# Optimization experiments

Measured on AMD Instinct MI355X. Metric: run time of the kernel, lower is better.

Reference implementation:

```python
import math
import jax, jax.numpy as jnp
import numpy as np


def setup_inputs() -> dict:
    key = jax.random.key(0)
    k1, k2 = jax.random.split(key)
    x = jax.random.normal(k1, (32, 3, 64, 64), dtype=jnp.float32)   # (B,C,H,W)
    y = jax.random.normal(k2, (512, 3, 64, 64), dtype=jnp.float32)  # (N,C,H,W)
    return {"x": x, "y": y}


def reference(x, y):
    # Faithful to torch rfft/irfft with normalized=True (unitary / 'ortho' scaling).
    B, C, H, W = x.shape
    scale = math.sqrt(H * W)  # self.N in the torch module
    X = jnp.fft.rfft2(x, norm="ortho")  # (B,C,H,W//2+1) complex
    Y = jnp.fft.rfft2(y, norm="ortho")  # (N,C,H,W//2+1) complex
    # conj(X) . Y summed over channels, fused as one complex contraction
    G = jnp.einsum("bchw,nchw->bnhw", jnp.conj(X), Y)  # (B,N,H,W//2+1)
    g = jnp.fft.irfft2(G, s=(H, W), norm="ortho") * scale  # (B,N,H,W)
    m = jnp.max(g, axis=(-2, -1))  # MaxPool2d(kernel=input_size) -> (B,N)
    xx = jnp.linalg.norm(x.reshape(B, -1), axis=-1)[:, None]  # (B,1)
    yy = jnp.linalg.norm(y.reshape(y.shape[0], -1), axis=-1)[None, :]  # (1,N)
    return m / xx / yy
```

## Files before the change

### kernel.cpp

```cpp
#include <hip/hip_runtime.h>
#include <math.h>

#define FBINS 2112
#define CSC 68

typedef float cplx __attribute__((ext_vector_type(2)));
typedef __fp16 half2v __attribute__((ext_vector_type(2)));
#define MK2(a,b) (cplx){(float)(a), (float)(b)}

__device__ __forceinline__ cplx shufxy(cplx a){ return __builtin_shufflevector(a, a, 1, 0); }
template<int S> __device__ __forceinline__ cplx imul(cplx a){
    return (S > 0) ? shufxy(a) * MK2(-1.f, 1.f) : shufxy(a) * MK2(1.f, -1.f);
}
template<int S> __device__ __forceinline__ cplx cmul_tw(cplx a, cplx w){
    cplx ws = shufxy(w);
    return (S > 0) ? a.x*w + a.y*(ws*MK2(-1.f, 1.f))
                   : a.x*(w*MK2(1.f, -1.f)) + a.y*ws;
}

__device__ __forceinline__ unsigned pack16(float a, float b){
    half2v h = __builtin_amdgcn_cvt_pkrtz(a, b);
    return __builtin_bit_cast(unsigned, h);
}
__device__ __forceinline__ half2v h2(unsigned u){ return __builtin_bit_cast(half2v, u); }
__device__ __forceinline__ float fdot2(half2v a, half2v b, float c){
#if __has_builtin(__builtin_amdgcn_fdot2)
    return __builtin_amdgcn_fdot2(a, b, c, false);
#else
    return c + (float)a.x*(float)b.x + (float)a.y*(float)b.y;
#endif
}

template<int S>
__device__ __forceinline__ void dft8(cplx v[8]) {
    const float C = 0.70710678118654752440f;
    cplx t0=v[0]+v[4], t4=v[0]-v[4];
    cplx t1=v[1]+v[5], t5=v[1]-v[5];
    cplx t2=v[2]+v[6], t6=v[2]-v[6];
    cplx t3=v[3]+v[7], t7=v[3]-v[7];
    cplx u0=t0+t2, u2=t0-t2;
    cplx u1=t1+t3, u3=t1-t3;
    v[0]=u0+u1; v[4]=u0-u1;
    cplx m3=imul<S>(u3);
    v[2]=u2+m3; v[6]=u2-m3;
    cplx z0=t4;
    cplx z1 = C*(t5 + imul<S>(t5));
    cplx z2 = imul<S>(t6);
    cplx z3 = C*(imul<S>(t7) - t7);
    cplx w0=z0+z2, w2=z0-z2;
    cplx w1=z1+z3, w3=z1-z3;
    v[1]=w0+w1; v[5]=w0-w1;
    cplx mb=imul<S>(w3);
    v[3]=w2+mb; v[7]=w2-mb;
}

template<int S>
__device__ __forceinline__ void fft64_from_regs(
    cplx v[8], cplx* __restrict__ mem, int base, int j, const cplx wj[7])
{
    dft8<S>(v);
    #pragma unroll
    for (int k=1;k<8;++k) v[k] = cmul_tw<S>(v[k], wj[k-1]);
    #pragma unroll
    for (int k=0;k<8;++k) mem[base + 8*j + (k^j)] = v[k];
    #pragma unroll
    for (int n=0;n<8;++n) v[n] = mem[base + 8*n + (j^n)];
    dft8<S>(v);
}

__device__ __forceinline__ void init_twtable(cplx* TWS, int tid){
    if (tid < 56) {
        int jj = tid / 7, kk = tid - 7*jj + 1;
        float sn, cs;
        sincosf(6.283185307179586f * (float)(jj*kk) / 64.0f, &sn, &cs);
        TWS[tid] = MK2(cs, sn);
    }
}
__device__ __forceinline__ void load_tw(const cplx* TWS, int j, cplx wj[7]){
    #pragma unroll
    for (int k=0;k<7;++k) wj[k] = TWS[j*7+k];
}

__global__ __launch_bounds__(256) void fwd_fft_kernel(
    const float* __restrict__ in, unsigned* __restrict__ oA,
    unsigned* __restrict__ oB, float* __restrict__ pn, int dual)
{
    __shared__ __align__(16) cplx CL[32*CSC + 64];
    __shared__ cplx TWS[56];
    __shared__ float red[4];
    const int tid = threadIdx.x, G = tid>>3, j = tid&7;

    init_twtable(TWS, tid);

    const float* img = in + (size_t)blockIdx.x * 4096;

    cplx wj[7];
    {
        cplx v[8];
        float ns = 0.f;
        #pragma unroll
        for (int nn=0;nn<8;++nn){ int w=8*nn+j;
            float a = img[64*G + w], c = img[64*(G+32) + w];
            v[nn] = MK2(a, c);
            ns = fmaf(a, a, ns); ns = fmaf(c, c, ns); }
        #pragma unroll
        for (int off = 32; off; off >>= 1) ns += __shfl_xor(ns, off);
        if ((tid & 63) == 0) red[tid >> 6] = ns;
        __syncthreads();
        load_tw(TWS, j, wj);
        int base = CSC*G;
        fft64_from_regs<-1>(v, CL, base, j, wj);
        #pragma unroll
        for (int k=0;k<8;++k) CL[base + j + 8*k] = v[k];
    }
    __syncthreads();

    {
        cplx v[8];
        if (G == 0) {
            #pragma unroll
            for (int nn=0;nn<8;++nn){
                int r=8*nn+j, p=r&31, hi=r>>5;
                cplx a0  = CL[CSC*p + 0];
                cplx a32 = CL[CSC*p + 32];
                v[nn] = hi ? MK2(a0.y, a32.y) : MK2(a0.x, a32.x);
            }
        } else {
            const int c = G;
            #pragma unroll
            for (int nn=0;nn<8;++nn){
                int r=8*nn+j, p=r&31, hi=r>>5;
                cplx A  = CL[CSC*p + c];
                cplx Bm = CL[CSC*p + 64 - c];
                if (!hi) v[nn] = 0.5f*(A + Bm*MK2(1.f,-1.f));
                else     v[nn] = 0.5f*(shufxy(A)*MK2(1.f,-1.f) + shufxy(Bm));
            }
        }
        __syncthreads();
        int base = CSC*G;
        fft64_from_regs<-1>(v, CL, base, j, wj);
        #pragma unroll
        for (int k=0;k<8;++k) CL[base + j + 8*k] = v[k];
    }
    __syncthreads();

    unsigned* a = oA + (size_t)blockIdx.x * FBINS;
    unsigned* bq = dual ? (oB + (size_t)blockIdx.x * FBINS) : nullptr;
    for (int i = tid; i < FBINS; i += 256) {
        int wp = i>>6, h = i&63;
        cplx r;
        if (wp == 0) {
            int h2i = (64-h)&63;
            cplx av = CL[h], bb = CL[h2i];
            r = 0.5f*(av + bb*MK2(1.f,-1.f));
        } else if (wp == 32) {
            int h2i = (64-h)&63;
            cplx av = CL[h], bb = CL[h2i];
            r = 0.5f*(shufxy(av)*MK2(1.f,-1.f) + shufxy(bb));
        } else {
            r = CL[CSC*wp + h];
        }
        a[i] = pack16(r.x, r.y);
        if (dual) bq[i] = pack16(-r.y, r.x);
    }
    if (tid == 0) pn[blockIdx.x] = red[0] + red[1] + red[2] + red[3];
}

__global__ __launch_bounds__(256) void corr_kernel(
    const unsigned* __restrict__ Xa, const unsigned* __restrict__ Xb,
    const unsigned* __restrict__ Yh,
    const float* __restrict__ px, const float* __restrict__ py,
    float* __restrict__ out)
{
    __shared__ __align__(16) cplx CL[32*CSC + 64];
    __shared__ cplx TWS[56];
    __shared__ float red[4];
    const int tid = threadIdx.x, G = tid>>3, j = tid&7;

    const int blk = blockIdx.x;
    const int xcd = blk & 7, idx = blk >> 3;
    const int n = xcd*64 + (idx & 63);
    const int b = idx >> 6;

    init_twtable(TWS, tid);

    const float x2 = px[3*b] + px[3*b+1] + px[3*b+2];
    const float y2 = py[3*n] + py[3*n+1] + py[3*n+2];
    const float dinv = rsqrtf(x2 * y2) * (1.0f/4096.0f);

    const uint4* pXa = (const uint4*)Xa + (size_t)b * 3 * 528;
    const uint4* pXb = (const uint4*)Xb + (size_t)b * 3 * 528;
    const uint4* pY  = (const uint4*)Yh + (size_t)n * 3 * 528;
    #pragma unroll
    for (int t = 0; t < 3; ++t) {
        int i = tid + (t<<8);
        if (i < 528) {
            float r0=0,i0=0,r1=0,i1=0,r2=0,i2=0,r3=0,i3=0;
            #pragma unroll
            for (int ch = 0; ch < 3; ++ch) {
                uint4 ua = pXa[ch*528 + i];
                uint4 ub = pXb[ch*528 + i];
                uint4 uy = pY [ch*528 + i];
                r0 = fdot2(h2(ua.x), h2(uy.x), r0);  i0 = fdot2(h2(ub.x), h2(uy.x), i0);
                r1 = fdot2(h2(ua.y), h2(uy.y), r1);  i1 = fdot2(h2(ub.y), h2(uy.y), i1);
                r2 = fdot2(h2(ua.z), h2(uy.z), r2);  i2 = fdot2(h2(ub.z), h2(uy.z), i2);
                r3 = fdot2(h2(ua.w), h2(uy.w), r3);  i3 = fdot2(h2(ub.w), h2(uy.w), i3);
            }
            int bin = 4*i;
            int s = CSC*(bin>>6) + (bin&63);
            *(float4*)&CL[s]   = make_float4(r0,i0,r1,i1);
            *(float4*)&CL[s+2] = make_float4(r2,i2,r3,i3);
        }
    }
    __syncthreads();

    cplx wj[7]; load_tw(TWS, j, wj);

    {
        cplx v[8];
        int base = CSC*G;
        if (G == 0) {
            #pragma unroll
            for (int nn=0;nn<8;++nn){
                int h = 8*nn + j;
                cplx a = CL[h];
                cplx c = CL[CSC*32 + h];
                v[nn] = a + imul<1>(c);
            }
        } else {
            #pragma unroll
            for (int nn=0;nn<8;++nn) v[nn] = CL[base + 8*nn + j];
        }
        fft64_from_regs<1>(v, CL, base, j, wj);
        #pragma unroll
        for (int k=0;k<8;++k) CL[base + j + 8*k] = v[k];
    }
    __syncthreads();

    float m = -3.4e38f;
    {
        const int r1 = G, r2 = G + 32;
        cplx v[8];
        if (j == 0) {
            cplx a = CL[r1], c = CL[r2];
            v[0] = MK2(a.x, c.x);
            v[4] = MK2(a.y, c.y);
        } else {
            cplx a = CL[CSC*j + r1], c = CL[CSC*j + r2];
            v[0] = a + imul<1>(c);
            int w2 = 32 - j;
            cplx a2 = CL[CSC*w2 + r1], c2 = CL[CSC*w2 + r2];
            v[4] = a2*MK2(1.f,-1.f) + shufxy(c2);
        }
        #pragma unroll
        for (int nn=1; nn<4; ++nn) {
            int w = 8*nn + j;
            cplx a = CL[CSC*w + r1], c = CL[CSC*w + r2];
            v[nn] = a + imul<1>(c);
        }
        #pragma unroll
        for (int nn=5; nn<8; ++nn) {
            int w2 = 64 - (8*nn + j);
            cplx a = CL[CSC*w2 + r1], c = CL[CSC*w2 + r2];
            v[nn] = a*MK2(1.f,-1.f) + shufxy(c);
        }
        __syncthreads();
        fft64_from_regs<1>(v, CL, CSC*G, j, wj);
        #pragma unroll
        for (int k=0;k<8;++k) m = fmaxf(m, fmaxf(v[k].x, v[k].y));
    }
    #pragma unroll
    for (int off = 32; off; off >>= 1) m = fmaxf(m, __shfl_xor(m, off));
    if ((tid & 63) == 0) red[tid >> 6] = m;
    __syncthreads();
    if (tid == 0) {
        float mm = fmaxf(fmaxf(red[0], red[1]), fmaxf(red[2], red[3]));
        out[b*512 + n] = mm * dinv;
    }
}

extern "C" void kernel_launch(void* const* d_in, const int* in_sizes, int n_in,
                              void* d_out, int out_size, void* d_ws, size_t ws_size,
                              hipStream_t stream) {
    const float* x = (const float*)d_in[0];
    const float* y = (const float*)d_in[1];
    float* out = (float*)d_out;

    unsigned* Xa = (unsigned*)d_ws;
    unsigned* Xb = Xa + 96 * FBINS;
    unsigned* Yh = Xb + 96 * FBINS;
    float* px = (float*)(Yh + 1536 * FBINS);
    float* py = px + 96;

    fwd_fft_kernel<<<96,   256, 0, stream>>>(x, Xa, Xb, px, 1);
    fwd_fft_kernel<<<1536, 256, 0, stream>>>(y, Yh, nullptr, py, 0);
    corr_kernel<<<16384, 256, 0, stream>>>(Xa, Xb, Yh, px, py, out);
}
```

Before: 96.30 us.

## Process four N images per block, keep X spectrum in registers, drop Xb buffer

Each correlation block now loops over four y-images for one x-image, holding the x spectrum in registers so it is loaded once and reused, and the grid shrinks by four. The separate conjugate-rotated X copy is removed; the imaginary part is computed with a swapped, sign-flipped Y word in a second fdot2. Shared-memory stride and the layout of the intermediate FFT output change to allow float4 accesses. This cuts global traffic and the per-block setup cost, but each block now runs its work serially, which lowers parallelism and lengthens each block.

```diff
diff --git a/kernel.cpp b/kernel.cpp
--- a/kernel.cpp
+++ b/kernel.cpp
@@ -2,7 +2,8 @@
 #include <math.h>
 
 #define FBINS 2112
-#define CSC 68
+#define CSC 66
+#define NPN 4
 
 typedef float cplx __attribute__((ext_vector_type(2)));
 typedef __fp16 half2v __attribute__((ext_vector_type(2)));
@@ -29,6 +30,11 @@
 #else
     return c + (float)a.x*(float)b.x + (float)a.y*(float)b.y;
 #endif
+}
+__device__ __forceinline__ void dotw(unsigned ux, unsigned uy, float& r, float& s){
+    unsigned ys = ((uy >> 16) | (uy << 16)) ^ 0x80000000u;
+    r = fdot2(h2(ux), h2(uy), r);
+    s = fdot2(h2(ux), h2(ys), s);
 }
 
 template<int S>
@@ -82,10 +88,10 @@
 }
 
 __global__ __launch_bounds__(256) void fwd_fft_kernel(
-    const float* __restrict__ in, unsigned* __restrict__ oA,
-    unsigned* __restrict__ oB, float* __restrict__ pn, int dual)
+    const float* __restrict__ in, unsigned* __restrict__ o,
+    float* __restrict__ pn)
 {
-    __shared__ __align__(16) cplx CL[32*CSC + 64];
+    __shared__ __align__(16) cplx CL[2176];
     __shared__ cplx TWS[56];
     __shared__ float red[4];
     const int tid = threadIdx.x, G = tid>>3, j = tid&7;
@@ -144,8 +150,7 @@
     }
     __syncthreads();
 
-    unsigned* a = oA + (size_t)blockIdx.x * FBINS;
-    unsigned* bq = dual ? (oB + (size_t)blockIdx.x * FBINS) : nullptr;
+    unsigned* a = o + (size_t)blockIdx.x * FBINS;
     for (int i = tid; i < FBINS; i += 256) {
         int wp = i>>6, h = i&63;
         cplx r;
@@ -161,121 +166,154 @@
             r = CL[CSC*wp + h];
         }
         a[i] = pack16(r.x, r.y);
-        if (dual) bq[i] = pack16(-r.y, r.x);
     }
     if (tid == 0) pn[blockIdx.x] = red[0] + red[1] + red[2] + red[3];
 }
 
 __global__ __launch_bounds__(256) void corr_kernel(
-    const unsigned* __restrict__ Xa, const unsigned* __restrict__ Xb,
-    const unsigned* __restrict__ Yh,
+    const unsigned* __restrict__ Xh, const unsigned* __restrict__ Yh,
     const float* __restrict__ px, const float* __restrict__ py,
     float* __restrict__ out)
 {
-    __shared__ __align__(16) cplx CL[32*CSC + 64];
+    __shared__ __align__(16) cplx CL[2176];
     __shared__ cplx TWS[56];
     __shared__ float red[4];
     const int tid = threadIdx.x, G = tid>>3, j = tid&7;
 
     const int blk = blockIdx.x;
     const int xcd = blk & 7, idx = blk >> 3;
-    const int n = xcd*64 + (idx & 63);
-    const int b = idx >> 6;
+    const int b  = idx >> 4;
+    const int n0 = xcd*64 + (idx & 15)*NPN;
 
     init_twtable(TWS, tid);
 
     const float x2 = px[3*b] + px[3*b+1] + px[3*b+2];
-    const float y2 = py[3*n] + py[3*n+1] + py[3*n+2];
-    const float dinv = rsqrtf(x2 * y2) * (1.0f/4096.0f);
-
-    const uint4* pXa = (const uint4*)Xa + (size_t)b * 3 * 528;
-    const uint4* pXb = (const uint4*)Xb + (size_t)b * 3 * 528;
-    const uint4* pY  = (const uint4*)Yh + (size_t)n * 3 * 528;
-    #pragma unroll
-    for (int t = 0; t < 3; ++t) {
-        int i = tid + (t<<8);
-        if (i < 528) {
-            float r0=0,i0=0,r1=0,i1=0,r2=0,i2=0,r3=0,i3=0;
-            #pragma unroll
-            for (int ch = 0; ch < 3; ++ch) {
-                uint4 ua = pXa[ch*528 + i];
-                uint4 ub = pXb[ch*528 + i];
-                uint4 uy = pY [ch*528 + i];
-                r0 = fdot2(h2(ua.x), h2(uy.x), r0);  i0 = fdot2(h2(ub.x), h2(uy.x), i0);
-                r1 = fdot2(h2(ua.y), h2(uy.y), r1);  i1 = fdot2(h2(ub.y), h2(uy.y), i1);
-                r2 = fdot2(h2(ua.z), h2(uy.z), r2);  i2 = fdot2(h2(ub.z), h2(uy.z), i2);
-                r3 = fdot2(h2(ua.w), h2(uy.w), r3);  i3 = fdot2(h2(ub.w), h2(uy.w), i3);
-            }
-            int bin = 4*i;
-            int s = CSC*(bin>>6) + (bin&63);
-            *(float4*)&CL[s]   = make_float4(r0,i0,r1,i1);
-            *(float4*)&CL[s+2] = make_float4(r2,i2,r3,i3);
-        }
-    }
+
+    const uint4* pX = (const uint4*)Xh + (size_t)b * 3 * 528;
+    uint4 xr[3][2];
+    #pragma unroll
+    for (int ch=0; ch<3; ++ch){
+        xr[ch][0] = pX[ch*528 + 2*tid];
+        xr[ch][1] = pX[ch*528 + 2*tid + 1];
+    }
+
     __syncthreads();
-
     cplx wj[7]; load_tw(TWS, j, wj);
 
-    {
-        cplx v[8];
-        int base = CSC*G;
-        if (G == 0) {
-            #pragma unroll
-            for (int nn=0;nn<8;++nn){
-                int h = 8*nn + j;
-                cplx a = CL[h];
-                cplx c = CL[CSC*32 + h];
-                v[nn] = a + imul<1>(c);
-            }
-        } else {
-            #pragma unroll
-            for (int nn=0;nn<8;++nn) v[nn] = CL[base + 8*nn + j];
-        }
-        fft64_from_regs<1>(v, CL, base, j, wj);
-        #pragma unroll
-        for (int k=0;k<8;++k) CL[base + j + 8*k] = v[k];
-    }
-    __syncthreads();
-
-    float m = -3.4e38f;
-    {
-        const int r1 = G, r2 = G + 32;
-        cplx v[8];
-        if (j == 0) {
-            cplx a = CL[r1], c = CL[r2];
-            v[0] = MK2(a.x, c.x);
-            v[4] = MK2(a.y, c.y);
-        } else {
-            cplx a = CL[CSC*j + r1], c = CL[CSC*j + r2];
-            v[0] = a + imul<1>(c);
-            int w2 = 32 - j;
-            cplx a2 = CL[CSC*w2 + r1], c2 = CL[CSC*w2 + r2];
-            v[4] = a2*MK2(1.f,-1.f) + shufxy(c2);
-        }
-        #pragma unroll
-        for (int nn=1; nn<4; ++nn) {
-            int w = 8*nn + j;
-            cplx a = CL[CSC*w + r1], c = CL[CSC*w + r2];
-            v[nn] = a + imul<1>(c);
-        }
-        #pragma unroll
-        for (int nn=5; nn<8; ++nn) {
-            int w2 = 64 - (8*nn + j);
-            cplx a = CL[CSC*w2 + r1], c = CL[CSC*w2 + r2];
-            v[nn] = a*MK2(1.f,-1.f) + shufxy(c);
-        }
-        __syncthreads();
-        fft64_from_regs<1>(v, CL, CSC*G, j, wj);
-        #pragma unroll
-        for (int k=0;k<8;++k) m = fmaxf(m, fmaxf(v[k].x, v[k].y));
-    }
-    #pragma unroll
-    for (int off = 32; off; off >>= 1) m = fmaxf(m, __shfl_xor(m, off));
-    if ((tid & 63) == 0) red[tid >> 6] = m;
-    __syncthreads();
-    if (tid == 0) {
-        float mm = fmaxf(fmaxf(red[0], red[1]), fmaxf(red[2], red[3]));
-        out[b*512 + n] = mm * dinv;
+    for (int q = 0; q < NPN; ++q) {
+        const int n = n0 + q;
+        const uint4* pY = (const uint4*)Yh + (size_t)n * 3 * 528;
+
+        {
+            float r[8], s[8];
+            #pragma unroll
+            for (int i=0;i<8;++i){ r[i]=0.f; s[i]=0.f; }
+            #pragma unroll
+            for (int ch=0; ch<3; ++ch){
+                uint4 y0 = pY[ch*528 + 2*tid];
+                uint4 y1 = pY[ch*528 + 2*tid + 1];
+                dotw(xr[ch][0].x, y0.x, r[0], s[0]);
+                dotw(xr[ch][0].y, y0.y, r[1], s[1]);
+                dotw(xr[ch][0].z, y0.z, r[2], s[2]);
+                dotw(xr[ch][0].w, y0.w, r[3], s[3]);
+                dotw(xr[ch][1].x, y1.x, r[4], s[4]);
+                dotw(xr[ch][1].y, y1.y, r[5], s[5]);
+                dotw(xr[ch][1].z, y1.z, r[6], s[6]);
+                dotw(xr[ch][1].w, y1.w, r[7], s[7]);
+            }
+            float4* dst = (float4*)&CL[CSC*G + 8*j];
+            #pragma unroll
+            for (int k=0;k<4;++k)
+                dst[k] = make_float4(r[2*k], s[2*k], r[2*k+1], s[2*k+1]);
+        }
+        if (tid < 8) {
+            float r[8], s[8];
+            #pragma unroll
+            for (int i=0;i<8;++i){ r[i]=0.f; s[i]=0.f; }
+            #pragma unroll
+            for (int ch=0; ch<3; ++ch){
+                uint4 x0 = pX[ch*528 + 512 + 2*tid];
+                uint4 x1 = pX[ch*528 + 512 + 2*tid + 1];
+                uint4 y0 = pY[ch*528 + 512 + 2*tid];
+                uint4 y1 = pY[ch*528 + 512 + 2*tid + 1];
+                dotw(x0.x, y0.x, r[0], s[0]);
+                dotw(x0.y, y0.y, r[1], s[1]);
+                dotw(x0.z, y0.z, r[2], s[2]);
+                dotw(x0.w, y0.w, r[3], s[3]);
+                dotw(x1.x, y1.x, r[4], s[4]);
+                dotw(x1.y, y1.y, r[5], s[5]);
+                dotw(x1.z, y1.z, r[6], s[6]);
+                dotw(x1.w, y1.w, r[7], s[7]);
+            }
+            float4* dst = (float4*)&CL[CSC*32 + 8*tid];
+            #pragma unroll
+            for (int k=0;k<4;++k)
+                dst[k] = make_float4(r[2*k], s[2*k], r[2*k+1], s[2*k+1]);
+        }
+        __syncthreads();
+
+        {
+            cplx v[8];
+            if (G == 0) {
+                #pragma unroll
+                for (int nn=0;nn<8;++nn){
+                    int h = 8*nn + j;
+                    cplx a = CL[h];
+                    cplx c = CL[CSC*32 + h];
+                    v[nn] = a + imul<1>(c);
+                }
+            } else {
+                #pragma unroll
+                for (int nn=0;nn<8;++nn) v[nn] = CL[CSC*G + 8*nn + j];
+            }
+            fft64_from_regs<1>(v, CL, CSC*G, j, wj);
+            #pragma unroll
+            for (int k=0;k<4;++k)
+                *(float4*)&CL[CSC*G + 2*(j+8*k)] =
+                    make_float4(v[k].x, v[k].y, v[k+4].x, v[k+4].y);
+        }
+        __syncthreads();
+
+        float m = -3.4e38f;
+        {
+            cplx v[8];
+            if (j == 0) {
+                float4 f = *(float4*)&CL[2*G];
+                v[0] = MK2(f.x, f.z);
+                v[4] = MK2(f.y, f.w);
+            } else {
+                float4 f = *(float4*)&CL[CSC*j + 2*G];
+                v[0] = MK2(f.x,f.y) + imul<1>(MK2(f.z,f.w));
+                float4 g2 = *(float4*)&CL[CSC*(32-j) + 2*G];
+                v[4] = MK2(g2.x,g2.y)*MK2(1.f,-1.f) + shufxy(MK2(g2.z,g2.w));
+            }
+            #pragma unroll
+            for (int nn=1;nn<4;++nn){
+                int w = 8*nn + j;
+                float4 f = *(float4*)&CL[CSC*w + 2*G];
+                v[nn] = MK2(f.x,f.y) + imul<1>(MK2(f.z,f.w));
+            }
+            #pragma unroll
+            for (int nn=5;nn<8;++nn){
+                int w2 = 64 - (8*nn + j);
+                float4 f = *(float4*)&CL[CSC*w2 + 2*G];
+                v[nn] = MK2(f.x,f.y)*MK2(1.f,-1.f) + shufxy(MK2(f.z,f.w));
+            }
+            __syncthreads();
+            fft64_from_regs<1>(v, CL, CSC*G, j, wj);
+            #pragma unroll
+            for (int k=0;k<8;++k) m = fmaxf(m, fmaxf(v[k].x, v[k].y));
+        }
+        #pragma unroll
+        for (int off = 32; off; off >>= 1) m = fmaxf(m, __shfl_xor(m, off));
+        if ((tid & 63) == 0) red[tid >> 6] = m;
+        __syncthreads();
+        if (tid == 0) {
+            const float y2 = py[3*n] + py[3*n+1] + py[3*n+2];
+            const float dinv = rsqrtf(x2 * y2) * (1.0f/4096.0f);
+            float mm = fmaxf(fmaxf(red[0], red[1]), fmaxf(red[2], red[3]));
+            out[b*512 + n] = mm * dinv;
+        }
     }
 }
 
@@ -286,13 +324,12 @@
     const float* y = (const float*)d_in[1];
     float* out = (float*)d_out;
 
-    unsigned* Xa = (unsigned*)d_ws;
-    unsigned* Xb = Xa + 96 * FBINS;
-    unsigned* Yh = Xb + 96 * FBINS;
+    unsigned* Xh = (unsigned*)d_ws;
+    unsigned* Yh = Xh + 96 * FBINS;
     float* px = (float*)(Yh + 1536 * FBINS);
     float* py = px + 96;
 
-    fwd_fft_kernel<<<96,   256, 0, stream>>>(x, Xa, Xb, px, 1);
-    fwd_fft_kernel<<<1536, 256, 0, stream>>>(y, Yh, nullptr, py, 0);
-    corr_kernel<<<16384, 256, 0, stream>>>(Xa, Xb, Yh, px, py, out);
-}
+    fwd_fft_kernel<<<96,   256, 0, stream>>>(x, Xh, px);
+    fwd_fft_kernel<<<1536, 256, 0, stream>>>(y, Yh, py);
+    corr_kernel<<<32*512/NPN, 256, 0, stream>>>(Xh, Yh, px, py, out);
+}
```

After: 119.5 us. +24.1%, slower.
